# Kernel tuning notes

Hardware: AMD Instinct MI355X
Metric: run time of the kernel (lower is better)

The kernel has to match this reference:

```python
import jax, jax.numpy as jnp
import numpy as np

N, E, F_IN, H, L, G = 50000, 800000, 128, 256, 64, 500


def setup_inputs() -> dict:
    key = jax.random.key(0)
    ks = jax.random.split(key, 12)
    s = 0.02
    x = jax.random.normal(ks[0], (N, F_IN), dtype=jnp.float32)
    edge_index = jax.random.randint(ks[1], (2, E), 0, N, dtype=jnp.int64 if jax.config.jax_enable_x64 else jnp.int32)
    batch = jnp.sort(jax.random.randint(ks[2], (N,), 0, G, dtype=jnp.int32))
    return {
        "x": x,
        "edge_index": edge_index,
        "batch": batch,
        "num_graphs": G,
        "W1": jax.random.normal(ks[3], (F_IN, H), dtype=jnp.float32) * s,
        "b1": jnp.zeros((H,), dtype=jnp.float32),
        "W2": jax.random.normal(ks[4], (H, H), dtype=jnp.float32) * s,
        "b2": jnp.zeros((H,), dtype=jnp.float32),
        "Wmu": jax.random.normal(ks[5], (H, L), dtype=jnp.float32) * s,
        "bmu": jnp.zeros((L,), dtype=jnp.float32),
        "Wlv": jax.random.normal(ks[6], (H, L), dtype=jnp.float32) * s,
        "blv": jnp.zeros((L,), dtype=jnp.float32),
    }


def _gcn_norm(edge_index, n_nodes):
    # PyG GCNConv default: add self-loops, symmetric normalization D^-1/2 A_hat D^-1/2
    loop = jnp.arange(n_nodes, dtype=edge_index.dtype)
    src = jnp.concatenate([edge_index[0], loop])
    dst = jnp.concatenate([edge_index[1], loop])
    deg = jax.ops.segment_sum(jnp.ones_like(dst, dtype=jnp.float32), dst, num_segments=n_nodes)
    dinv = jnp.where(deg > 0, jax.lax.rsqrt(deg), 0.0)
    norm = dinv[src] * dinv[dst]  # [E + N]
    return src, dst, norm


def _gcn_conv(h, src, dst, norm, W, b, n_nodes):
    h = h @ W                              # [N, out]
    msg = norm[:, None] * h[src]           # gather + scale: [E+N, out]
    agg = jax.ops.segment_sum(msg, dst, num_segments=n_nodes)  # scatter-add
    return agg + b


def reference(x, edge_index, batch, num_graphs, W1, b1, W2, b2, Wmu, bmu, Wlv, blv):
    n_nodes = x.shape[0]
    src, dst, norm = _gcn_norm(edge_index, n_nodes)
    h = jax.nn.relu(_gcn_conv(x, src, dst, norm, W1, b1, n_nodes))
    h = jax.nn.relu(_gcn_conv(h, src, dst, norm, W2, b2, n_nodes))
    # global_mean_pool over batch ids
    sums = jax.ops.segment_sum(h, batch, num_segments=num_graphs)       # [G, H]
    cnt = jax.ops.segment_sum(jnp.ones((n_nodes,), h.dtype), batch, num_segments=num_graphs)
    h_graph = sums / jnp.maximum(cnt, 1.0)[:, None]
    mu = h_graph @ Wmu + bmu
    logvar = h_graph @ Wlv + blv
    return mu, logvar
```

## Files before the change

kernel.cpp:

```cpp
#include <hip/hip_runtime.h>
#include <hip/hip_fp16.h>

#define N_NODES 50000
#define N_EDGES 800000
#define F_IN_D  128
#define H_DIM   256
#define L_DIM   64
#define G_NUM   500

typedef unsigned int   u32;
typedef unsigned short u16;
typedef unsigned char  u8;
typedef __attribute__((ext_vector_type(8))) short short8;
typedef __attribute__((ext_vector_type(4))) float f32x4;
typedef __attribute__((ext_vector_type(2))) float f32x2;

#define CUR_STRIDE 16

static __device__ __forceinline__ float bf2f(u16 u) {
    union { u32 i; float f; } x; x.i = ((u32)u) << 16; return x.f;
}
static __device__ __forceinline__ u16 f2bf(float f) {
    union { float f; u32 i; } x; x.f = f;
    u32 r = (x.i + 0x7fffu + ((x.i >> 16) & 1u)) >> 16;
    return (u16)r;
}
static __device__ __forceinline__ float edge_w(u32 e) {
    return __half2float(__ushort_as_half((u16)(e >> 16)));
}

static __device__ __forceinline__ u32 pack4_fp8(u32 a, u32 b) {
    u32 w = __builtin_amdgcn_cvt_pk_fp8_f32(bf2f((u16)(a & 0xffff)),
                                            bf2f((u16)(a >> 16)), 0, false);
    w = __builtin_amdgcn_cvt_pk_fp8_f32(bf2f((u16)(b & 0xffff)),
                                        bf2f((u16)(b >> 16)), w, true);
    return w;
}

static __device__ __forceinline__ u32 bswz_idx(int n, int k, int plane, int KS) {
    int n0g = n >> 6, nt = (n >> 4) & 3, lr = n & 15;
    int k0i = k >> 5, ks = k & 31, lq = ks >> 3, j = ks & 7;
    return ((u32)((((n0g * KS + k0i) * 2 + plane) * 4 + nt) * 64 + lq * 16 + lr)) * 8 + j;
}

#define NXQ (N_NODES * F_IN_D / 4)
#define NW1 (F_IN_D * H_DIM)
#define NW2 (H_DIM * H_DIM)
#define NB_COUNT ((N_EDGES + 255) / 256)
#define NB_SCAN  ((N_NODES + 255) / 256)
#define NB_CONV  ((NXQ + NW1 + NW2 + 255) / 256)

__global__ void prep_kernel(const int* __restrict__ dst, int* __restrict__ hist,
                            const int* __restrict__ batch, int* __restrict__ goff,
                            const float* __restrict__ x, u16* __restrict__ xb,
                            const float* __restrict__ W1, u16* __restrict__ w1swz,
                            const float* __restrict__ W2, u16* __restrict__ w2swz) {
    int b = blockIdx.x;
    if (b < NB_COUNT) {
        int i = b * 256 + threadIdx.x;
        if (i < N_EDGES) atomicAdd(&hist[dst[i]], 1);
    } else if (b < NB_COUNT + NB_SCAN) {
        int i = (b - NB_COUNT) * 256 + threadIdx.x;
        if (i >= N_NODES) return;
        int v = batch[i];
        if (i == 0) {
            for (int g = 0; g <= v; ++g) goff[g] = 0;
        } else {
            int p = batch[i - 1];
            for (int g = p + 1; g <= v; ++g) goff[g] = i;
        }
        if (i == N_NODES - 1) {
            for (int g = v + 1; g <= G_NUM; ++g) goff[g] = N_NODES;
        }
    } else {
        int i = (b - NB_COUNT - NB_SCAN) * 256 + threadIdx.x;
        if (i < NXQ) {
            float4 v = *(const float4*)&x[(size_t)i * 4];
            ushort4 o;
            o.x = f2bf(v.x); o.y = f2bf(v.y); o.z = f2bf(v.z); o.w = f2bf(v.w);
            *(ushort4*)&xb[(size_t)i * 4] = o;
        } else if (i < NXQ + NW1) {
            int idx = i - NXQ;
            int k = idx >> 8, n = idx & 255;
            float w = W1[idx];
            u16 h = f2bf(w);
            w1swz[bswz_idx(n, k, 0, F_IN_D / 32)] = h;
            w1swz[bswz_idx(n, k, 1, F_IN_D / 32)] = f2bf(w - bf2f(h));
        } else if (i < NXQ + NW1 + NW2) {
            int idx = i - NXQ - NW1;
            int k = idx >> 8, n = idx & 255;
            float w = W2[idx];
            u16 h = f2bf(w);
            w2swz[bswz_idx(n, k, 0, H_DIM / 32)] = h;
            w2swz[bswz_idx(n, k, 1, H_DIM / 32)] = f2bf(w - bf2f(h));
        }
    }
}

__global__ void scan_chunk_kernel(const int* __restrict__ in, int* __restrict__ excl,
                                  int* __restrict__ partials, float* __restrict__ dinv, int n) {
    __shared__ int sm[256];
    int t = threadIdx.x;
    int i = blockIdx.x * 256 + t;
    int v = (i < n) ? in[i] : 0;
    sm[t] = v; __syncthreads();
    for (int off = 1; off < 256; off <<= 1) {
        int x = (t >= off) ? sm[t - off] : 0;
        __syncthreads();
        sm[t] += x;
        __syncthreads();
    }
    if (i < n) {
        excl[i] = sm[t] - v;
        dinv[i] = 1.0f / sqrtf((float)(v + 1));
    }
    if (t == 255) partials[blockIdx.x] = sm[255];
}

__global__ void scan_final_kernel(const int* __restrict__ excl, const int* __restrict__ partials,
                                  int* __restrict__ out, int* __restrict__ cursor, int n, int nb) {
    __shared__ int sm[256];
    int t = threadIdx.x;
    int v = (t < nb) ? partials[t] : 0;
    sm[t] = v; __syncthreads();
    for (int off = 1; off < 256; off <<= 1) {
        int x = (t >= off) ? sm[t - off] : 0;
        __syncthreads();
        sm[t] += x;
        __syncthreads();
    }
    int pre = (blockIdx.x > 0) ? sm[blockIdx.x - 1] : 0;
    int i = blockIdx.x * 256 + t;
    if (i < n) {
        int val = excl[i] + pre;
        out[i] = val;
        cursor[(size_t)i * CUR_STRIDE] = val;
    }
    if (blockIdx.x == (unsigned)(nb - 1) && t == 0) out[n] = sm[nb - 1];
}

__global__ __launch_bounds__(256)
void place_kernel(const int* __restrict__ src, const int* __restrict__ dst,
                  const float* __restrict__ dinv,
                  int* __restrict__ cursor, u32* __restrict__ csr) {
    int e = blockIdx.x * 256 + threadIdx.x;
    if (e < N_EDGES) {
        int s = src[e];
        int d = dst[e];
        float di = dinv[s];
        int pos = atomicAdd(&cursor[(size_t)d * CUR_STRIDE], 1);
        u32 h = (u32)__half_as_ushort(__float2half(di));
        csr[pos] = (u32)s | (h << 16);
    }
}

__global__ __launch_bounds__(256)
void agg128_kernel(const u16* __restrict__ In, const float* __restrict__ dinv,
                   const int* __restrict__ rp, const u32* __restrict__ csr,
                   u16* __restrict__ Out) {
    int node = blockIdx.x * 4 + (threadIdx.x >> 6);
    int lane = threadIdx.x & 63;
    if (node >= N_NODES) return;
    int c = lane * 2;
    float di = dinv[node];
    int r0 = rp[node], r1 = rp[node + 1];
    u32 sv = *(const u32*)&In[(size_t)node * 128 + c];
    float a0 = di * bf2f((u16)(sv & 0xffff));
    float a1 = di * bf2f((u16)(sv >> 16));
    int j = r0;
    for (; j + 8 <= r1; j += 8) {
        u32 e[8];
        u32 v[8];
#pragma unroll
        for (int q = 0; q < 8; ++q) e[q] = csr[j + q];
#pragma unroll
        for (int q = 0; q < 8; ++q) v[q] = *(const u32*)&In[(size_t)(e[q] & 0xffff) * 128 + c];
#pragma unroll
        for (int q = 0; q < 8; ++q) {
            float w = edge_w(e[q]);
            a0 = fmaf(w, bf2f((u16)(v[q] & 0xffff)), a0);
            a1 = fmaf(w, bf2f((u16)(v[q] >> 16)), a1);
        }
    }
    for (; j + 4 <= r1; j += 4) {
        u32 e[4];
        u32 v[4];
#pragma unroll
        for (int q = 0; q < 4; ++q) e[q] = csr[j + q];
#pragma unroll
        for (int q = 0; q < 4; ++q) v[q] = *(const u32*)&In[(size_t)(e[q] & 0xffff) * 128 + c];
#pragma unroll
        for (int q = 0; q < 4; ++q) {
            float w = edge_w(e[q]);
            a0 = fmaf(w, bf2f((u16)(v[q] & 0xffff)), a0);
            a1 = fmaf(w, bf2f((u16)(v[q] >> 16)), a1);
        }
    }
    for (; j < r1; ++j) {
        u32 e = csr[j];
        u32 v = *(const u32*)&In[(size_t)(e & 0xffff) * 128 + c];
        float w = edge_w(e);
        a0 = fmaf(w, bf2f((u16)(v & 0xffff)), a0);
        a1 = fmaf(w, bf2f((u16)(v >> 16)), a1);
    }
    u32 o = ((u32)f2bf(di * a1) << 16) | (u32)f2bf(di * a0);
    *(u32*)&Out[(size_t)node * 128 + c] = o;
}

__global__ __launch_bounds__(256)
void agg256_fp8_kernel(const u8* __restrict__ In, const float* __restrict__ dinv,
                       const int* __restrict__ rp, const u32* __restrict__ csr,
                       u16* __restrict__ Out) {
    int node = blockIdx.x * 4 + (threadIdx.x >> 6);
    int lane = threadIdx.x & 63;
    if (node >= N_NODES) return;
    int c = lane * 4;
    float di = dinv[node];
    int r0 = rp[node], r1 = rp[node + 1];
    u32 sv = *(const u32*)&In[(size_t)node * 256 + c];
    f32x2 s01 = __builtin_amdgcn_cvt_pk_f32_fp8(sv, false);
    f32x2 s23 = __builtin_amdgcn_cvt_pk_f32_fp8(sv, true);
    float a0 = di * s01.x;
    float a1 = di * s01.y;
    float a2 = di * s23.x;
    float a3 = di * s23.y;
    int j = r0;
    for (; j + 8 <= r1; j += 8) {
        u32 e[8];
        u32 v[8];
#pragma unroll
        for (int q = 0; q < 8; ++q) e[q] = csr[j + q];
#pragma unroll
        for (int q = 0; q < 8; ++q) v[q] = *(const u32*)&In[(size_t)(e[q] & 0xffff) * 256 + c];
#pragma unroll
        for (int q = 0; q < 8; ++q) {
            float w = edge_w(e[q]);
            f32x2 p0 = __builtin_amdgcn_cvt_pk_f32_fp8(v[q], false);
            f32x2 p1 = __builtin_amdgcn_cvt_pk_f32_fp8(v[q], true);
            a0 = fmaf(w, p0.x, a0);
            a1 = fmaf(w, p0.y, a1);
            a2 = fmaf(w, p1.x, a2);
            a3 = fmaf(w, p1.y, a3);
        }
    }
    for (; j + 4 <= r1; j += 4) {
        u32 e[4];
        u32 v[4];
#pragma unroll
        for (int q = 0; q < 4; ++q) e[q] = csr[j + q];
#pragma unroll
        for (int q = 0; q < 4; ++q) v[q] = *(const u32*)&In[(size_t)(e[q] & 0xffff) * 256 + c];
#pragma unroll
        for (int q = 0; q < 4; ++q) {
            float w = edge_w(e[q]);
            f32x2 p0 = __builtin_amdgcn_cvt_pk_f32_fp8(v[q], false);
            f32x2 p1 = __builtin_amdgcn_cvt_pk_f32_fp8(v[q], true);
            a0 = fmaf(w, p0.x, a0);
            a1 = fmaf(w, p0.y, a1);
            a2 = fmaf(w, p1.x, a2);
            a3 = fmaf(w, p1.y, a3);
        }
    }
    for (; j < r1; ++j) {
        u32 e = csr[j];
        u32 v = *(const u32*)&In[(size_t)(e & 0xffff) * 256 + c];
        float w = edge_w(e);
        f32x2 p0 = __builtin_amdgcn_cvt_pk_f32_fp8(v, false);
        f32x2 p1 = __builtin_amdgcn_cvt_pk_f32_fp8(v, true);
        a0 = fmaf(w, p0.x, a0);
        a1 = fmaf(w, p0.y, a1);
        a2 = fmaf(w, p1.x, a2);
        a3 = fmaf(w, p1.y, a3);
    }
    uint2 o;
    o.x = ((u32)f2bf(di * a1) << 16) | (u32)f2bf(di * a0);
    o.y = ((u32)f2bf(di * a3) << 16) | (u32)f2bf(di * a2);
    *(uint2*)&Out[(size_t)node * 256 + c] = o;
}

template<int K>
__global__ __launch_bounds__(256, 3)
void gemm1_kernel(const u16* __restrict__ A, const short8* __restrict__ Bswz,
                  const float* __restrict__ bias, u8* __restrict__ Out, int M) {
    const int KS = K / 32;
    __shared__ u16 cst[64][264];
    int tid  = threadIdx.x;
    int wave = tid >> 6, lane = tid & 63;
    int m0 = blockIdx.x * 64;
    int n0 = wave * 64;
    int lr = lane & 15;
    int lk = (lane >> 4) * 8;

    f32x4 acc[4][4];
#pragma unroll
    for (int i = 0; i < 4; ++i)
#pragma unroll
        for (int j = 0; j < 4; ++j) acc[i][j] = {0.f, 0.f, 0.f, 0.f};

    for (int k0i = 0; k0i < KS; ++k0i) {
        int k0 = k0i * 32;
        short8 a[4], bh[4], bl[4];
#pragma unroll
        for (int mt = 0; mt < 4; ++mt) {
            int m = m0 + mt * 16 + lr;
            if (m > M - 1) m = M - 1;
            a[mt] = *(const short8*)&A[(size_t)m * K + k0 + lk];
        }
        const short8* bp = Bswz + ((size_t)(wave * KS + k0i) * 8) * 64 + lane;
#pragma unroll
        for (int nt = 0; nt < 4; ++nt) {
            bh[nt] = bp[(size_t)nt * 64];
            bl[nt] = bp[(size_t)(4 + nt) * 64];
        }
#pragma unroll
        for (int mt = 0; mt < 4; ++mt)
#pragma unroll
            for (int nt = 0; nt < 4; ++nt) {
                acc[mt][nt] = __builtin_amdgcn_mfma_f32_16x16x32_bf16(a[mt], bh[nt], acc[mt][nt], 0, 0, 0);
                acc[mt][nt] = __builtin_amdgcn_mfma_f32_16x16x32_bf16(a[mt], bl[nt], acc[mt][nt], 0, 0, 0);
            }
    }

#pragma unroll
    for (int mt = 0; mt < 4; ++mt)
#pragma unroll
        for (int nt = 0; nt < 4; ++nt) {
            int col = n0 + nt * 16 + lr;
            float b = bias[col];
#pragma unroll
            for (int r = 0; r < 4; ++r) {
                int row = mt * 16 + (lane >> 4) * 4 + r;
                cst[row][col] = f2bf(fmaxf(acc[mt][nt][r] + b, 0.f));
            }
        }
    __syncthreads();
#pragma unroll
    for (int p = 0; p < 8; ++p) {
        int row = p * 8 + (tid >> 5);
        int c16 = (tid & 31) * 8;
        int m = m0 + row;
        if (m < M) {
            uint4 v = *(const uint4*)&cst[row][c16];
            uint2 o = make_uint2(pack4_fp8(v.x, v.y), pack4_fp8(v.z, v.w));
            *(uint2*)&Out[(size_t)m * 256 + c16] = o;
        }
    }
}

__global__ __launch_bounds__(256, 3)
void gemm2_pool_kernel(const u16* __restrict__ A, const short8* __restrict__ Bswz,
                       const float* __restrict__ bias, const int* __restrict__ batch,
                       float* __restrict__ pooled, int M) {
    const int K = H_DIM, KS = K / 32;
    __shared__ u16 cst[64][264];
    __shared__ int batch_s[64];
    int tid  = threadIdx.x;
    int wave = tid >> 6, lane = tid & 63;
    int m0 = blockIdx.x * 64;
    int n0 = wave * 64;
    int lr = lane & 15;
    int lk = (lane >> 4) * 8;

    f32x4 acc[4][4];
#pragma unroll
    for (int i = 0; i < 4; ++i)
#pragma unroll
        for (int j = 0; j < 4; ++j) acc[i][j] = {0.f, 0.f, 0.f, 0.f};

    for (int k0i = 0; k0i < KS; ++k0i) {
        int k0 = k0i * 32;
        short8 a[4], bh[4], bl[4];
#pragma unroll
        for (int mt = 0; mt < 4; ++mt) {
            int m = m0 + mt * 16 + lr;
            if (m > M - 1) m = M - 1;
            a[mt] = *(const short8*)&A[(size_t)m * K + k0 + lk];
        }
        const short8* bp = Bswz + ((size_t)(wave * KS + k0i) * 8) * 64 + lane;
#pragma unroll
        for (int nt = 0; nt < 4; ++nt) {
            bh[nt] = bp[(size_t)nt * 64];
            bl[nt] = bp[(size_t)(4 + nt) * 64];
        }
#pragma unroll
        for (int mt = 0; mt < 4; ++mt)
#pragma unroll
            for (int nt = 0; nt < 4; ++nt) {
                acc[mt][nt] = __builtin_amdgcn_mfma_f32_16x16x32_bf16(a[mt], bh[nt], acc[mt][nt], 0, 0, 0);
                acc[mt][nt] = __builtin_amdgcn_mfma_f32_16x16x32_bf16(a[mt], bl[nt], acc[mt][nt], 0, 0, 0);
            }
    }

    if (tid < 64) {
        int m = m0 + tid;
        batch_s[tid] = (m < M) ? batch[m] : -1;
    }
#pragma unroll
    for (int mt = 0; mt < 4; ++mt)
#pragma unroll
        for (int nt = 0; nt < 4; ++nt) {
            int col = n0 + nt * 16 + lr;
            float b = bias[col];
#pragma unroll
            for (int r = 0; r < 4; ++r) {
                int row = mt * 16 + (lane >> 4) * 4 + r;
                cst[row][col] = f2bf(fmaxf(acc[mt][nt][r] + b, 0.f));
            }
        }
    __syncthreads();

    int rows = M - m0; if (rows > 64) rows = 64;
    float s = 0.f;
    int gp = batch_s[0];
    for (int r = 0; r < rows; ++r) {
        int g = batch_s[r];
        if (g != gp) {
            atomicAdd(&pooled[(size_t)gp * H_DIM + tid], s);
            s = 0.f;
            gp = g;
        }
        s += bf2f(cst[r][tid]);
    }
    atomicAdd(&pooled[(size_t)gp * H_DIM + tid], s);
}

__global__ void head_kernel(const float* __restrict__ pooled, const int* __restrict__ goff,
                            const float* __restrict__ Wmu, const float* __restrict__ bmu,
                            const float* __restrict__ Wlv, const float* __restrict__ blv,
                            float* __restrict__ out) {
    __shared__ float hg[H_DIM];
    int g = blockIdx.x, l = threadIdx.x;
    float inv = 1.0f / fmaxf((float)(goff[g + 1] - goff[g]), 1.0f);
    for (int k = l; k < H_DIM; k += 64) hg[k] = pooled[(size_t)g * H_DIM + k] * inv;
    __syncthreads();
    float mu = bmu[l], lv = blv[l];
    for (int k = 0; k < H_DIM; ++k) {
        float h = hg[k];
        mu = fmaf(h, Wmu[k * L_DIM + l], mu);
        lv = fmaf(h, Wlv[k * L_DIM + l], lv);
    }
    out[(size_t)g * L_DIM + l] = mu;
    out[(size_t)G_NUM * L_DIM + (size_t)g * L_DIM + l] = lv;
}

extern "C" void kernel_launch(void* const* d_in, const int* in_sizes, int n_in,
                              void* d_out, int out_size, void* d_ws, size_t ws_size,
                              hipStream_t stream) {
    const float* x     = (const float*)d_in[0];
    const int*   ei    = (const int*)  d_in[1];
    const int*   batch = (const int*)  d_in[2];
    const float* W1  = (const float*)d_in[4];
    const float* b1  = (const float*)d_in[5];
    const float* W2  = (const float*)d_in[6];
    const float* b2  = (const float*)d_in[7];
    const float* Wmu = (const float*)d_in[8];
    const float* bmu = (const float*)d_in[9];
    const float* Wlv = (const float*)d_in[10];
    const float* blv = (const float*)d_in[11];
    const int* src = ei;
    const int* dst = ei + N_EDGES;

    char* ws = (char*)d_ws;
    size_t off = 0;
    auto alloc = [&](size_t bytes) -> void* {
        void* p = ws + off;
        off += (bytes + 255) & ~(size_t)255;
        return p;
    };
    int*   hist     = (int*)alloc((size_t)N_NODES * 4);
    float* pooled   = (float*)alloc((size_t)G_NUM * H_DIM * 4);
    float* dinv     = (float*)alloc((size_t)N_NODES * 4);
    int*   row_ptr  = (int*)alloc((size_t)(N_NODES + 1) * 4);
    int*   cursor   = (int*)alloc((size_t)N_NODES * 4 * CUR_STRIDE);
    u32*   csr      = (u32*)alloc((size_t)N_EDGES * 4);
    int*   excl     = (int*)alloc((size_t)N_NODES * 4);
    int*   partials = (int*)alloc(256 * 4);
    int*   goff     = (int*)alloc((size_t)(G_NUM + 1) * 4);
    u16*   xb    = (u16*)alloc((size_t)N_NODES * F_IN_D * 2);
    u16*   Xa    = (u16*)alloc((size_t)N_NODES * F_IN_D * 2);
    u8*    H8    = (u8*)alloc((size_t)N_NODES * H_DIM);
    u16*   Ha    = (u16*)alloc((size_t)N_NODES * H_DIM * 2);
    u16*   w1swz = (u16*)alloc((size_t)2 * F_IN_D * H_DIM * 2);
    u16*   w2swz = (u16*)alloc((size_t)2 * H_DIM * H_DIM * 2);
    (void)ws_size; (void)n_in; (void)in_sizes; (void)out_size;

    const int GEMM_NB = (N_NODES + 63) / 64;
    size_t zero_bytes = (size_t)((char*)(pooled + G_NUM * H_DIM) - (char*)hist);

    hipMemsetAsync(hist, 0, zero_bytes, stream);
    prep_kernel<<<NB_COUNT + NB_SCAN + NB_CONV, 256, 0, stream>>>(
        dst, hist, batch, goff, x, xb, W1, w1swz, W2, w2swz);
    scan_chunk_kernel<<<NB_SCAN, 256, 0, stream>>>(hist, excl, partials, dinv, N_NODES);
    scan_final_kernel<<<NB_SCAN, 256, 0, stream>>>(excl, partials, row_ptr, cursor, N_NODES, NB_SCAN);
    place_kernel<<<(N_EDGES + 255) / 256, 256, 0, stream>>>(src, dst, dinv, cursor, csr);

    agg128_kernel<<<(N_NODES + 3) / 4, 256, 0, stream>>>(xb, dinv, row_ptr, csr, Xa);
    gemm1_kernel<F_IN_D><<<GEMM_NB, 256, 0, stream>>>(Xa, (const short8*)w1swz, b1, H8, N_NODES);
    agg256_fp8_kernel<<<(N_NODES + 3) / 4, 256, 0, stream>>>(H8, dinv, row_ptr, csr, Ha);
    gemm2_pool_kernel<<<GEMM_NB, 256, 0, stream>>>(Ha, (const short8*)w2swz, b2, batch, pooled, N_NODES);

    head_kernel<<<G_NUM, 64, 0, stream>>>(pooled, goff, Wmu, bmu, Wlv, blv, (float*)d_out);
}
```

Before: 309.8 us.

## Build CSR via two-pass bucketed binning instead of per-edge global atomics

Replaces the single place kernel, which did one global atomicAdd per edge on a strided per-node cursor, with two kernels. The first bins edges into 256-node buckets using shared-memory histograms and one global atomic per bucket per block. The second scatters each bucket into its final CSR slots using shared-memory cursors. This cuts global atomic contention and scattered writes, at the cost of an extra launch and an 8-byte intermediate record per edge that is written and read back.

```diff
diff --git a/kernel.cpp b/kernel.cpp
--- a/kernel.cpp
+++ b/kernel.cpp
@@ -15,7 +15,11 @@
 typedef __attribute__((ext_vector_type(4))) float f32x4;
 typedef __attribute__((ext_vector_type(2))) float f32x2;
 
+#define BSHIFT 8
+#define NBUCK ((N_NODES + 255) >> BSHIFT)
 #define CUR_STRIDE 16
+#define BIN_NB 512
+#define EPB ((N_EDGES + BIN_NB - 1) / BIN_NB)
 
 static __device__ __forceinline__ float bf2f(u16 u) {
     union { u32 i; float f; } x; x.i = ((u32)u) << 16; return x.f;
@@ -118,7 +122,7 @@
 }
 
 __global__ void scan_final_kernel(const int* __restrict__ excl, const int* __restrict__ partials,
-                                  int* __restrict__ out, int* __restrict__ cursor, int n, int nb) {
+                                  int* __restrict__ out, int* __restrict__ bcur, int n, int nb) {
     __shared__ int sm[256];
     int t = threadIdx.x;
     int v = (t < nb) ? partials[t] : 0;
@@ -134,23 +138,55 @@
     if (i < n) {
         int val = excl[i] + pre;
         out[i] = val;
-        cursor[(size_t)i * CUR_STRIDE] = val;
+        if ((i & 255) == 0) bcur[(i >> BSHIFT) * CUR_STRIDE] = val;
     }
     if (blockIdx.x == (unsigned)(nb - 1) && t == 0) out[n] = sm[nb - 1];
 }
 
 __global__ __launch_bounds__(256)
-void place_kernel(const int* __restrict__ src, const int* __restrict__ dst,
-                  const float* __restrict__ dinv,
-                  int* __restrict__ cursor, u32* __restrict__ csr) {
-    int e = blockIdx.x * 256 + threadIdx.x;
-    if (e < N_EDGES) {
-        int s = src[e];
-        int d = dst[e];
-        float di = dinv[s];
-        int pos = atomicAdd(&cursor[(size_t)d * CUR_STRIDE], 1);
-        u32 h = (u32)__half_as_ushort(__float2half(di));
-        csr[pos] = (u32)s | (h << 16);
+void bin_kernel(const int* __restrict__ src, const int* __restrict__ dst,
+                const float* __restrict__ dinv,
+                int* __restrict__ bcur, uint2* __restrict__ binrec) {
+    __shared__ int lhist[NBUCK];
+    __shared__ int lbase[NBUCK];
+    int t = threadIdx.x;
+    int e0 = blockIdx.x * EPB;
+    int e1 = e0 + EPB; if (e1 > N_EDGES) e1 = N_EDGES;
+    for (int i = t; i < NBUCK; i += 256) lhist[i] = 0;
+    __syncthreads();
+    for (int e = e0 + t; e < e1; e += 256)
+        atomicAdd(&lhist[dst[e] >> BSHIFT], 1);
+    __syncthreads();
+    for (int i = t; i < NBUCK; i += 256) {
+        int c = lhist[i];
+        lbase[i] = c ? atomicAdd(&bcur[i * CUR_STRIDE], c) : 0;
+        lhist[i] = 0;
+    }
+    __syncthreads();
+    for (int e = e0 + t; e < e1; e += 256) {
+        int d = dst[e], s = src[e];
+        int bkt = d >> BSHIFT;
+        int rank = atomicAdd(&lhist[bkt], 1);
+        u32 w = (u32)__half_as_ushort(__float2half(dinv[s]));
+        binrec[(size_t)lbase[bkt] + rank] = make_uint2((u32)s | (w << 16), (u32)(d & 255));
+    }
+}
+
+__global__ __launch_bounds__(256)
+void grp_kernel(const int* __restrict__ rp, const uint2* __restrict__ binrec,
+                u32* __restrict__ csr) {
+    __shared__ int ncur[256];
+    int b = blockIdx.x;
+    int t = threadIdx.x;
+    int n0 = b << BSHIFT;
+    int n1 = n0 + 256; if (n1 > N_NODES) n1 = N_NODES;
+    if (n0 + t < n1) ncur[t] = rp[n0 + t];
+    __syncthreads();
+    int s0 = rp[n0], s1 = rp[n1];
+    for (int p = s0 + t; p < s1; p += 256) {
+        uint2 r = binrec[p];
+        int pos = atomicAdd(&ncur[r.y], 1);
+        csr[pos] = r.x;
     }
 }
 
@@ -471,8 +507,9 @@
     float* pooled   = (float*)alloc((size_t)G_NUM * H_DIM * 4);
     float* dinv     = (float*)alloc((size_t)N_NODES * 4);
     int*   row_ptr  = (int*)alloc((size_t)(N_NODES + 1) * 4);
-    int*   cursor   = (int*)alloc((size_t)N_NODES * 4 * CUR_STRIDE);
+    int*   bcur     = (int*)alloc((size_t)NBUCK * CUR_STRIDE * 4);
     u32*   csr      = (u32*)alloc((size_t)N_EDGES * 4);
+    uint2* binrec   = (uint2*)alloc((size_t)N_EDGES * 8);
     int*   excl     = (int*)alloc((size_t)N_NODES * 4);
     int*   partials = (int*)alloc(256 * 4);
     int*   goff     = (int*)alloc((size_t)(G_NUM + 1) * 4);
@@ -491,8 +528,9 @@
     prep_kernel<<<NB_COUNT + NB_SCAN + NB_CONV, 256, 0, stream>>>(
         dst, hist, batch, goff, x, xb, W1, w1swz, W2, w2swz);
     scan_chunk_kernel<<<NB_SCAN, 256, 0, stream>>>(hist, excl, partials, dinv, N_NODES);
-    scan_final_kernel<<<NB_SCAN, 256, 0, stream>>>(excl, partials, row_ptr, cursor, N_NODES, NB_SCAN);
-    place_kernel<<<(N_EDGES + 255) / 256, 256, 0, stream>>>(src, dst, dinv, cursor, csr);
+    scan_final_kernel<<<NB_SCAN, 256, 0, stream>>>(excl, partials, row_ptr, bcur, N_NODES, NB_SCAN);
+    bin_kernel<<<BIN_NB, 256, 0, stream>>>(src, dst, dinv, bcur, binrec);
+    grp_kernel<<<NBUCK, 256, 0, stream>>>(row_ptr, binrec, csr);
 
     agg128_kernel<<<(N_NODES + 3) / 4, 256, 0, stream>>>(xb, dinv, row_ptr, csr, Xa);
     gemm1_kernel<F_IN_D><<<GEMM_NB, 256, 0, stream>>>(Xa, (const short8*)w1swz, b1, H8, N_NODES);
```

Result: faster. 298.4 us (-3.7%).
